# Performance work log

Measured on AMD Instinct MI355X. Metric: run time of the kernel, lower is better.

Reference implementation:

```python
import jax, jax.numpy as jnp
import numpy as np

B, S, T, D, H_HEADS = 2, 2048, 2048, 1024, 16
HD = D // H_HEADS
EPS = 1e-5


def _ln(x, g, b):
    m = jnp.mean(x, axis=-1, keepdims=True)
    v = jnp.mean(jnp.square(x - m), axis=-1, keepdims=True)
    return g * (x - m) * jax.lax.rsqrt(v + EPS) + b


def _mha(xq, xkv, Wq, bq, Wk, bk, Wv, bv, Wo, bo, causal):
    Bq, Lq, _ = xq.shape
    Lk = xkv.shape[1]
    q = (xq @ Wq + bq).reshape(Bq, Lq, H_HEADS, HD)
    k = (xkv @ Wk + bk).reshape(Bq, Lk, H_HEADS, HD)
    v = (xkv @ Wv + bv).reshape(Bq, Lk, H_HEADS, HD)
    scores = jnp.einsum('bqhd,bkhd->bhqk', q, k) / jnp.sqrt(jnp.asarray(HD, q.dtype))
    if causal:
        mask = jnp.tril(jnp.ones((Lq, Lk), dtype=bool))
        scores = jnp.where(mask, scores, jnp.asarray(-1e9, scores.dtype))
    p = jax.nn.softmax(scores, axis=-1)
    o = jnp.einsum('bhqk,bkhd->bqhd', p, v).reshape(Bq, Lq, D)
    return o @ Wo + bo


def setup_inputs() -> dict:
    key = jax.random.key(0)
    ks = jax.random.split(key, 24)
    s = 0.02
    def w(i):
        return jax.random.normal(ks[i], (D, D), jnp.float32) * s
    inp = {
        'S0': jax.random.normal(ks[20], (B, S, D), jnp.float32),
        'H': jax.random.normal(ks[21], (B, T, D), jnp.float32),
        'Wq1': w(0), 'bq1': jnp.zeros((D,)), 'Wk1': w(1), 'bk1': jnp.zeros((D,)),
        'Wv1': w(2), 'bv1': jnp.zeros((D,)), 'Wo1': w(3), 'bo1': jnp.zeros((D,)),
        'ln1_g': jnp.ones((D,)), 'ln1_b': jnp.zeros((D,)),
        'Wq2': w(4), 'bq2': jnp.zeros((D,)), 'Wk2': w(5), 'bk2': jnp.zeros((D,)),
        'Wv2': w(6), 'bv2': jnp.zeros((D,)), 'Wo2': w(7), 'bo2': jnp.zeros((D,)),
        'ln2_g': jnp.ones((D,)), 'ln2_b': jnp.zeros((D,)),
        'Wf': w(8), 'bf': jnp.zeros((D,)),
        'ln3_g': jnp.ones((D,)), 'ln3_b': jnp.zeros((D,)),
    }
    return inp


def reference(S0, H, Wq1, bq1, Wk1, bk1, Wv1, bv1, Wo1, bo1, ln1_g, ln1_b,
              Wq2, bq2, Wk2, bk2, Wv2, bv2, Wo2, bo2, ln2_g, ln2_b,
              Wf, bf, ln3_g, ln3_b):
    # masked (causal) self-attention + add&norm
    a1 = _mha(S0, S0, Wq1, bq1, Wk1, bk1, Wv1, bv1, Wo1, bo1, causal=True)
    S1 = _ln(S0 + a1, ln1_g, ln1_b)
    # cross-attention over encoder output H + add&norm
    a2 = _mha(S1, H, Wq2, bq2, Wk2, bk2, Wv2, bv2, Wo2, bo2, causal=False)
    S2 = _ln(S1 + a2, ln2_g, ln2_b)
    # FFN (single Linear) + add&norm
    S3 = _ln(S2 + (S2 @ Wf + bf), ln3_g, ln3_b)
    return S3
```

## Files before the change

kernel.cpp:

```cpp
#include <hip/hip_runtime.h>
#include <hip/hip_bf16.h>
#include <cstdint>
#include <cstddef>


#define D_DIM 1024
#define SEQ   2048
#define NHEAD 16
#define HDIM  64
#define MROWS 4096

typedef __attribute__((ext_vector_type(8)))  short bf16x8;
typedef __attribute__((ext_vector_type(4)))  float f32x4;
typedef __attribute__((ext_vector_type(16))) float f32x16;
typedef __attribute__((ext_vector_type(4)))  unsigned int u32x4;

static __device__ __forceinline__ short f2bf(float x) {
    __hip_bfloat16 h = __float2bfloat16(x);
    return *reinterpret_cast<short*>(&h);
}

static __device__ __forceinline__ unsigned int cvtpk(float lo, float hi2) {
    unsigned int r;
    asm("v_cvt_pk_bf16_f32 %0, %1, %2" : "=v"(r) : "v"(lo), "v"(hi2));
    return r;
}

#define GLOAD_LDS16(g, l)                                                     \
    __builtin_amdgcn_global_load_lds(                                         \
        (const __attribute__((address_space(1))) unsigned int*)(g),           \
        (__attribute__((address_space(3))) unsigned int*)(l), 16, 0, 0)

struct WPtrs { const float* p[9]; };

__global__ __launch_bounds__(256) void transpose_conv_kernel(
    WPtrs wp, short* __restrict__ Wt)
{
    __shared__ float tl[64][65];
    const int t = threadIdx.x;
    const float* src = wp.p[blockIdx.z];
    short* dst = Wt + (size_t)blockIdx.z * D_DIM * D_DIM;
    const int r0 = blockIdx.x * 64;
    const int c0 = blockIdx.y * 64;
    #pragma unroll
    for (int i = 0; i < 4; ++i) {
        int row = i * 16 + (t >> 4);
        int col = (t & 15) * 4;
        float4 v = *(const float4*)(src + (size_t)(r0 + row) * D_DIM + c0 + col);
        tl[row][col + 0] = v.x; tl[row][col + 1] = v.y;
        tl[row][col + 2] = v.z; tl[row][col + 3] = v.w;
    }
    __syncthreads();
    #pragma unroll
    for (int i = 0; i < 4; ++i) {
        int nrow = i * 16 + (t >> 4);
        int kcol = (t & 15) * 4;
        ushort4 o;
        o.x = (unsigned short)f2bf(tl[kcol + 0][nrow]);
        o.y = (unsigned short)f2bf(tl[kcol + 1][nrow]);
        o.z = (unsigned short)f2bf(tl[kcol + 2][nrow]);
        o.w = (unsigned short)f2bf(tl[kcol + 3][nrow]);
        *(ushort4*)(dst + (size_t)(c0 + nrow) * D_DIM + r0 + kcol) = o;
    }
}

__global__ __launch_bounds__(256) void conv2_kernel(
    const float* __restrict__ s0, const float* __restrict__ hx,
    short* __restrict__ d0, short* __restrict__ d1)
{
    const bool second = blockIdx.x >= 2048;
    const float* src = second ? hx : s0;
    short* dst = second ? d1 : d0;
    size_t i = ((size_t)(blockIdx.x - (second ? 2048 : 0)) * 256 + threadIdx.x) * 8;
    float4 a = *(const float4*)(src + i);
    float4 b = *(const float4*)(src + i + 4);
    bf16x8 o;
    o[0] = f2bf(a.x); o[1] = f2bf(a.y); o[2] = f2bf(a.z); o[3] = f2bf(a.w);
    o[4] = f2bf(b.x); o[5] = f2bf(b.y); o[6] = f2bf(b.z); o[7] = f2bf(b.w);
    *(bf16x8*)(dst + i) = o;
}

__global__ __launch_bounds__(256) void bias_concat_kernel(
    const float* __restrict__ bq1, const float* __restrict__ bk1,
    const float* __restrict__ bv1, const float* __restrict__ bk2,
    const float* __restrict__ bv2, float* __restrict__ cb1,
    float* __restrict__ cb2)
{
    const int i = blockIdx.x * 256 + threadIdx.x;
    if      (i < 1024) cb1[i] = bq1[i];
    else if (i < 2048) cb1[i] = bk1[i - 1024];
    else if (i < 3072) cb1[i] = bv1[i - 2048];
    else if (i < 4096) cb2[i - 3072] = bk2[i - 3072];
    else               cb2[i - 3072] = bv2[i - 4096];
}

__device__ __forceinline__ void gemm_qkv_body(
    short* __restrict__ As_, short* __restrict__ Bs_,
    const short* __restrict__ A, const short* __restrict__ Bt,
    const float* __restrict__ bias,
    short* __restrict__ Qh, short* __restrict__ Kh, short* __restrict__ Vh,
    int col0, float qscale, int bx, int by)
{
    const int t = threadIdx.x;
    const int wave = t >> 6, lane = t & 63;
    const int wm = wave >> 1, wn = wave & 1;
    const int m0 = bx * 128, n0 = by * 128;
    const int l15 = lane & 15, l4 = lane >> 4;
    const int lrow = lane >> 2, lcol = (lane & 3) * 8;
    f32x4 acc[4][4] = {};
    for (int k0 = 0; k0 < D_DIM; k0 += 32) {
        __syncthreads();
        #pragma unroll
        for (int c = 0; c < 2; ++c) {
            int chunk = wave + c * 4;
            int row = chunk * 16 + lrow;
            GLOAD_LDS16(A  + (size_t)(m0 + row) * D_DIM + k0 + lcol,
                        As_ + chunk * 512 + lane * 8);
            GLOAD_LDS16(Bt + (size_t)(n0 + row) * D_DIM + k0 + lcol,
                        Bs_ + chunk * 512 + lane * 8);
        }
        __syncthreads();
        bf16x8 af[4], bfr[4];
        const int kq = l4 * 8;
        #pragma unroll
        for (int i = 0; i < 4; ++i)
            af[i] = *(const bf16x8*)&As_[(wm * 64 + i * 16 + l15) * 32 + kq];
        #pragma unroll
        for (int j = 0; j < 4; ++j)
            bfr[j] = *(const bf16x8*)&Bs_[(wn * 64 + j * 16 + l15) * 32 + kq];
        #pragma unroll
        for (int i = 0; i < 4; ++i)
            #pragma unroll
            for (int j = 0; j < 4; ++j)
                acc[i][j] = __builtin_amdgcn_mfma_f32_16x16x32_bf16(
                    af[i], bfr[j], acc[i][j], 0, 0, 0);
    }
    const int rbase = m0 + wm * 64;
    const int cbase = n0 + wn * 64;
    float bv[4];
    #pragma unroll
    for (int j = 0; j < 4; ++j) bv[j] = bias[cbase + j * 16 + l15];
    #pragma unroll
    for (int i = 0; i < 4; ++i) {
        #pragma unroll
        for (int r = 0; r < 4; ++r) {
            const int grow = rbase + i * 16 + l4 * 4 + r;
            const int b = grow >> 11, s = grow & 2047;
            #pragma unroll
            for (int j = 0; j < 4; ++j) {
                const int vcol = col0 + cbase + j * 16 + l15;
                float v = acc[i][j][r] + bv[j];
                if (vcol < 1024) v *= qscale;
                short* dst = (vcol < 1024) ? Qh : ((vcol < 2048) ? Kh : Vh);
                const int h = (vcol >> 6) & 15, hd = vcol & 63;
                dst[((size_t)(b * 16 + h) * SEQ + s) * HDIM + hd] = f2bf(v);
            }
        }
    }
}

__global__ __launch_bounds__(256) void gemm_qkv_kernel(
    const short* __restrict__ A, const short* __restrict__ Bt,
    const float* __restrict__ bias,
    short* __restrict__ Qh, short* __restrict__ Kh, short* __restrict__ Vh,
    int col0, float qscale)
{
    __shared__ short lds[8192];
    gemm_qkv_body(lds, lds + 4096, A, Bt, bias, Qh, Kh, Vh,
                  col0, qscale, blockIdx.x, blockIdx.y);
}

__global__ __launch_bounds__(256) void gemm_resid_kernel(
    const short* __restrict__ A, const short* __restrict__ Bt,
    const float* __restrict__ bias, const float* __restrict__ resid,
    float* __restrict__ Cout)
{
    __shared__ short As[128 * 32];
    __shared__ short Bs[64 * 32];
    const int t = threadIdx.x;
    const int wave = t >> 6, lane = t & 63;
    const int wm = wave >> 1, wn = wave & 1;
    const int m0 = blockIdx.x * 128, n0 = blockIdx.y * 64;
    const int l15 = lane & 15, l4 = lane >> 4;
    const int lrow = lane >> 2, lcol = (lane & 3) * 8;
    f32x4 acc[4][2] = {};
    for (int k0 = 0; k0 < D_DIM; k0 += 32) {
        __syncthreads();
        #pragma unroll
        for (int c = 0; c < 2; ++c) {
            int chunk = wave + c * 4;
            int row = chunk * 16 + lrow;
            GLOAD_LDS16(A + (size_t)(m0 + row) * D_DIM + k0 + lcol,
                        As + chunk * 512 + lane * 8);
        }
        {
            int row = wave * 16 + lrow;
            GLOAD_LDS16(Bt + (size_t)(n0 + row) * D_DIM + k0 + lcol,
                        Bs + wave * 512 + lane * 8);
        }
        __syncthreads();
        bf16x8 af[4], bfr[2];
        const int kq = l4 * 8;
        #pragma unroll
        for (int i = 0; i < 4; ++i)
            af[i] = *(const bf16x8*)&As[(wm * 64 + i * 16 + l15) * 32 + kq];
        #pragma unroll
        for (int j = 0; j < 2; ++j)
            bfr[j] = *(const bf16x8*)&Bs[(wn * 32 + j * 16 + l15) * 32 + kq];
        #pragma unroll
        for (int i = 0; i < 4; ++i)
            #pragma unroll
            for (int j = 0; j < 2; ++j)
                acc[i][j] = __builtin_amdgcn_mfma_f32_16x16x32_bf16(
                    af[i], bfr[j], acc[i][j], 0, 0, 0);
    }
    const int rbase = m0 + wm * 64;
    const int cbase = n0 + wn * 32;
    float bv[2];
    #pragma unroll
    for (int j = 0; j < 2; ++j) bv[j] = bias[cbase + j * 16 + l15];
    #pragma unroll
    for (int i = 0; i < 4; ++i) {
        #pragma unroll
        for (int r = 0; r < 4; ++r) {
            const int grow = rbase + i * 16 + l4 * 4 + r;
            #pragma unroll
            for (int j = 0; j < 2; ++j) {
                const int gcol = cbase + j * 16 + l15;
                float v = acc[i][j][r] + bv[j]
                        + resid[(size_t)grow * D_DIM + gcol];
                Cout[(size_t)grow * D_DIM + gcol] = v;
            }
        }
    }
}

template<bool CAUSAL>
__device__ __forceinline__ void attn_body(
    char* ldsb,
    const short* __restrict__ Qh, const short* __restrict__ Kh,
    const short* __restrict__ Vh, short* __restrict__ O, const int id)
{
    const int t = threadIdx.x, wave = t >> 6, lane = t & 63;
    const int q_own = lane & 31, hi = lane >> 5;
    const int bh = ((id & 7) << 2) | ((id >> 3) & 3);
    const int qsel = id >> 5;
    const int b = bh >> 4, h = bh & 15;
    const short* Qp = Qh + (size_t)bh * SEQ * HDIM;
    const short* Kp = Kh + (size_t)bh * SEQ * HDIM;
    const short* Vp = Vh + (size_t)bh * SEQ * HDIM;
    short* Op = O + (size_t)b * SEQ * D_DIM + h * HDIM;

    const int ksrc = (t & 7) ^ ((t >> 3) & 7);
    const int vr2 = (t & 31) * 2, vg = (t >> 5) * 8;
    const int swz = (q_own & 7) << 3;

    const int npm = CAUSAL ? 2 : 1;
    for (int pm = 0; pm < npm; ++pm) {
        const int qt = CAUSAL ? (pm == 0 ? qsel : 15 - qsel) : qsel;
        const int q0 = qt * 128;
        const int qw = q0 + wave * 32;

        bf16x8 qf[4];
        #pragma unroll
        for (int s = 0; s < 4; ++s)
            qf[s] = *(const bf16x8*)(Qp + (size_t)(qw + q_own) * HDIM
                                     + s * 16 + hi * 8);

        int qkb[4], pvb[8], vwb[8], kgb;
        #pragma unroll
        for (int s = 0; s < 4; ++s)
            qkb[s] = q_own * 128 + 2 * ((s * 16 + hi * 8) ^ swz);
        #pragma unroll
        for (int ks = 0; ks < 8; ++ks)
            pvb[ks] = 32768 + q_own * 256 + 2 * ((ks * 16 + hi * 8) ^ swz);
        #pragma unroll
        for (int j = 0; j < 8; ++j)
            vwb[j] = 32768 + (vg + j) * 256 + 2 * (vr2 ^ (j << 3));
        kgb = t * 16;

        f32x16 oacc[2] = {};
        float m_ = -3e38f, l_ = 0.f;
        const int nkt = CAUSAL ? (qt + 1) : (SEQ / 128);

        bf16x8 va0, vb0, va1, vb1;

        if (pm) __syncthreads();

        #pragma unroll
        for (int c = 0; c < 4; ++c) {
            const int row = c * 32 + (t >> 3);
            GLOAD_LDS16(Kp + (size_t)row * HDIM + ksrc * 8,
                        ldsb + kgb + c * 4096);
        }
        va0 = *(const bf16x8*)(Vp + (size_t)vr2 * HDIM + vg);
        vb0 = *(const bf16x8*)(Vp + (size_t)(vr2 + 1) * HDIM + vg);
        va1 = *(const bf16x8*)(Vp + (size_t)(64 + vr2) * HDIM + vg);
        vb1 = *(const bf16x8*)(Vp + (size_t)(65 + vr2) * HDIM + vg);
        #pragma unroll
        for (int j = 0; j < 8; ++j) {
            unsigned int p0 = ((unsigned int)(unsigned short)vb0[j] << 16)
                            | (unsigned short)va0[j];
            unsigned int p1 = ((unsigned int)(unsigned short)vb1[j] << 16)
                            | (unsigned short)va1[j];
            *(unsigned int*)(ldsb + vwb[j])       = p0;
            *(unsigned int*)(ldsb + vwb[j] + 128) = p1;
        }
        __syncthreads();
        kgb ^= 16384;
        #pragma unroll
        for (int j = 0; j < 8; ++j) vwb[j] ^= 16384;

        for (int kt = 0; kt < nkt; ++kt) {
            const int kbase = kt * 128;
            const bool have_next = (kt + 1 < nkt);

            if (have_next) {
                #pragma unroll
                for (int c = 0; c < 4; ++c) {
                    const int row = kbase + 128 + c * 32 + (t >> 3);
                    GLOAD_LDS16(Kp + (size_t)row * HDIM + ksrc * 8,
                                ldsb + kgb + c * 4096);
                }
                va0 = *(const bf16x8*)(Vp + (size_t)(kbase + 128 + vr2) * HDIM + vg);
                vb0 = *(const bf16x8*)(Vp + (size_t)(kbase + 129 + vr2) * HDIM + vg);
                va1 = *(const bf16x8*)(Vp + (size_t)(kbase + 192 + vr2) * HDIM + vg);
                vb1 = *(const bf16x8*)(Vp + (size_t)(kbase + 193 + vr2) * HDIM + vg);
            }

            f32x16 sc[4] = {};
            __builtin_amdgcn_s_setprio(1);
            #pragma unroll
            for (int kt2 = 0; kt2 < 4; ++kt2) {
                #pragma unroll
                for (int s = 0; s < 4; ++s) {
                    bf16x8 kf = *(const bf16x8*)(ldsb + qkb[s] + kt2 * 4096);
                    sc[kt2] = __builtin_amdgcn_mfma_f32_32x32x16_bf16(
                        kf, qf[s], sc[kt2], 0, 0, 0);
                }
            }
            __builtin_amdgcn_s_setprio(0);

            if (CAUSAL && (kbase + 127 > qw)) {
                #pragma unroll
                for (int kt2 = 0; kt2 < 4; ++kt2)
                    #pragma unroll
                    for (int rr = 0; rr < 16; ++rr) {
                        const int k = kbase + kt2 * 32
                                    + (rr & 3) + 8 * (rr >> 2) + 4 * hi;
                        if (k > qw + q_own) sc[kt2][rr] = -1e30f;
                    }
            }

            float km[4];
            #pragma unroll
            for (int kt2 = 0; kt2 < 4; ++kt2) {
                float t0 = fmaxf(fmaxf(sc[kt2][0],  sc[kt2][1]),  sc[kt2][2]);
                float t1 = fmaxf(fmaxf(sc[kt2][3],  sc[kt2][4]),  sc[kt2][5]);
                float t2 = fmaxf(fmaxf(sc[kt2][6],  sc[kt2][7]),  sc[kt2][8]);
                float t3 = fmaxf(fmaxf(sc[kt2][9],  sc[kt2][10]), sc[kt2][11]);
                float t4 = fmaxf(fmaxf(sc[kt2][12], sc[kt2][13]), sc[kt2][14]);
                float u  = fmaxf(fmaxf(t0, t1), t2);
                float v  = fmaxf(fmaxf(t3, t4), sc[kt2][15]);
                km[kt2] = fmaxf(u, v);
            }
            float pmax = fmaxf(fmaxf(fmaxf(km[0], km[1]), km[2]), km[3]);
            pmax = fmaxf(pmax, __shfl_xor(pmax, 32));

            if (!__all(pmax - m_ <= 8.0f)) {
                const float mnew = fmaxf(m_, pmax);
                const float corr = exp2f(m_ - mnew);
                l_ *= corr;
                #pragma unroll
                for (int ht = 0; ht < 2; ++ht)
                    #pragma unroll
                    for (int rr = 0; rr < 16; ++rr)
                        oacc[ht][rr] *= corr;
                m_ = mnew;
            }

            float s_own = 0.f;
            #pragma unroll
            for (int kt2 = 0; kt2 < 4; ++kt2) {
                float t0 = 0.f, t1 = 0.f, t2 = 0.f, t3 = 0.f;
                #pragma unroll
                for (int rr = 0; rr < 4; ++rr) {
                    float a  = exp2f(sc[kt2][rr]      - m_);
                    float b2 = exp2f(sc[kt2][4 + rr]  - m_);
                    float c  = exp2f(sc[kt2][8 + rr]  - m_);
                    float d  = exp2f(sc[kt2][12 + rr] - m_);
                    sc[kt2][rr] = a;      t0 += a;
                    sc[kt2][4 + rr] = b2; t1 += b2;
                    sc[kt2][8 + rr] = c;  t2 += c;
                    sc[kt2][12 + rr] = d; t3 += d;
                }
                s_own += (t0 + t1) + (t2 + t3);
            }
            l_ += s_own + __shfl_xor(s_own, 32);

            u32x4 paw[8];
            #pragma unroll
            for (int kt2 = 0; kt2 < 4; ++kt2) {
                unsigned int w0a = cvtpk(sc[kt2][0],  sc[kt2][1]);
                unsigned int w0b = cvtpk(sc[kt2][2],  sc[kt2][3]);
                unsigned int w1a = cvtpk(sc[kt2][4],  sc[kt2][5]);
                unsigned int w1b = cvtpk(sc[kt2][6],  sc[kt2][7]);
                unsigned int w2a = cvtpk(sc[kt2][8],  sc[kt2][9]);
                unsigned int w2b = cvtpk(sc[kt2][10], sc[kt2][11]);
                unsigned int w3a = cvtpk(sc[kt2][12], sc[kt2][13]);
                unsigned int w3b = cvtpk(sc[kt2][14], sc[kt2][15]);
                asm("v_permlane32_swap_b32 %0, %1" : "+v"(w0a), "+v"(w1a));
                asm("v_permlane32_swap_b32 %0, %1" : "+v"(w0b), "+v"(w1b));
                asm("v_permlane32_swap_b32 %0, %1" : "+v"(w2a), "+v"(w3a));
                asm("v_permlane32_swap_b32 %0, %1" : "+v"(w2b), "+v"(w3b));
                paw[kt2 * 2 + 0][0] = w0a; paw[kt2 * 2 + 0][1] = w0b;
                paw[kt2 * 2 + 0][2] = w1a; paw[kt2 * 2 + 0][3] = w1b;
                paw[kt2 * 2 + 1][0] = w2a; paw[kt2 * 2 + 1][1] = w2b;
                paw[kt2 * 2 + 1][2] = w3a; paw[kt2 * 2 + 1][3] = w3b;
            }

            __builtin_amdgcn_s_setprio(1);
            #pragma unroll
            for (int ht = 0; ht < 2; ++ht) {
                #pragma unroll
                for (int ks = 0; ks < 8; ++ks) {
                    bf16x8 vf = *(const bf16x8*)(ldsb + pvb[ks] + ht * 8192);
                    union { u32x4 u; bf16x8 bv8; } pc;
                    pc.u = paw[ks];
                    oacc[ht] = __builtin_amdgcn_mfma_f32_32x32x16_bf16(
                        vf, pc.bv8, oacc[ht], 0, 0, 0);
                }
            }
            __builtin_amdgcn_s_setprio(0);

            if (have_next) {
                #pragma unroll
                for (int j = 0; j < 8; ++j) {
                    unsigned int p0 = ((unsigned int)(unsigned short)vb0[j] << 16)
                                    | (unsigned short)va0[j];
                    unsigned int p1 = ((unsigned int)(unsigned short)vb1[j] << 16)
                                    | (unsigned short)va1[j];
                    *(unsigned int*)(ldsb + vwb[j])       = p0;
                    *(unsigned int*)(ldsb + vwb[j] + 128) = p1;
                }
                __syncthreads();
            }
            kgb ^= 16384;
            #pragma unroll
            for (int s = 0; s < 4; ++s) qkb[s] ^= 16384;
            #pragma unroll
            for (int ks = 0; ks < 8; ++ks) pvb[ks] ^= 16384;
            #pragma unroll
            for (int j = 0; j < 8; ++j) vwb[j] ^= 16384;
        }

        const float inv = 1.0f / l_;
        const int grow = qw + q_own;
        #pragma unroll
        for (int ht = 0; ht < 2; ++ht)
            #pragma unroll
            for (int j = 0; j < 4; ++j) {
                ushort4 o;
                o.x = (unsigned short)f2bf(oacc[ht][4 * j + 0] * inv);
                o.y = (unsigned short)f2bf(oacc[ht][4 * j + 1] * inv);
                o.z = (unsigned short)f2bf(oacc[ht][4 * j + 2] * inv);
                o.w = (unsigned short)f2bf(oacc[ht][4 * j + 3] * inv);
                *(ushort4*)&Op[(size_t)grow * D_DIM + ht * 32 + 8 * j + 4 * hi] = o;
            }
    }
}

template<bool CAUSAL>
__global__ __launch_bounds__(256, 2) void attn_mfma_kernel(
    const short* __restrict__ Qh, const short* __restrict__ Kh,
    const short* __restrict__ Vh, short* __restrict__ O)
{
    __shared__ short lds[32768];
    attn_body<CAUSAL>((char*)lds, Qh, Kh, Vh, O, blockIdx.x);
}

__global__ __launch_bounds__(256, 2) void fused_cattn_kv2_kernel(
    const short* __restrict__ Qh, const short* __restrict__ Kh,
    const short* __restrict__ Vh, short* __restrict__ O,
    const short* __restrict__ A2, const short* __restrict__ Bt2,
    const float* __restrict__ bias2,
    short* __restrict__ Kh2, short* __restrict__ Vh2)
{
    __shared__ short lds[32768];
    if (blockIdx.x < 256) {
        attn_body<true>((char*)lds, Qh, Kh, Vh, O, blockIdx.x);
    } else {
        const int bx2 = blockIdx.x - 256;
        gemm_qkv_body(lds, lds + 4096, A2, Bt2, bias2,
                      nullptr, Kh2, Vh2, 1024, 1.0f, bx2 & 31, bx2 >> 5);
    }
}

__global__ __launch_bounds__(256) void ln_kernel(
    const float* __restrict__ X, const float* __restrict__ g,
    const float* __restrict__ bb, float* __restrict__ outf,
    short* __restrict__ outb)
{
    const int row = blockIdx.x;
    const int t = threadIdx.x;
    const float* x = X + (size_t)row * D_DIM;
    float4 v = *(const float4*)(x + (t << 2));
    float s  = v.x + v.y + v.z + v.w;
    float sq = v.x * v.x + v.y * v.y + v.z * v.z + v.w * v.w;
    #pragma unroll
    for (int off = 1; off < 64; off <<= 1) {
        s  += __shfl_xor(s, off);
        sq += __shfl_xor(sq, off);
    }
    __shared__ float ss[4], ssq[4];
    const int wid = t >> 6, lane = t & 63;
    if (lane == 0) { ss[wid] = s; ssq[wid] = sq; }
    __syncthreads();
    s  = ss[0] + ss[1] + ss[2] + ss[3];
    sq = ssq[0] + ssq[1] + ssq[2] + ssq[3];
    const float mean = s * (1.0f / 1024.0f);
    const float var  = sq * (1.0f / 1024.0f) - mean * mean;
    const float inv  = rsqrtf(var + 1e-5f);
    float4 gv = *(const float4*)(g  + (t << 2));
    float4 bv = *(const float4*)(bb + (t << 2));
    float4 o;
    o.x = gv.x * (v.x - mean) * inv + bv.x;
    o.y = gv.y * (v.y - mean) * inv + bv.y;
    o.z = gv.z * (v.z - mean) * inv + bv.z;
    o.w = gv.w * (v.w - mean) * inv + bv.w;
    if (outf) *(float4*)(outf + (size_t)row * D_DIM + (t << 2)) = o;
    if (outb) {
        ushort4 ob;
        ob.x = (unsigned short)f2bf(o.x); ob.y = (unsigned short)f2bf(o.y);
        ob.z = (unsigned short)f2bf(o.z); ob.w = (unsigned short)f2bf(o.w);
        *(ushort4*)(outb + (size_t)row * D_DIM + (t << 2)) = ob;
    }
}

extern "C" void kernel_launch(void* const* d_in, const int* in_sizes, int n_in,
                              void* d_out, int out_size, void* d_ws, size_t ws_size,
                              hipStream_t stream)
{
    (void)in_sizes; (void)n_in; (void)out_size; (void)ws_size;
    const float* S0f = (const float*)d_in[0];
    const float* Hf  = (const float*)d_in[1];
    const float* bq1 = (const float*)d_in[3];
    const float* bk1 = (const float*)d_in[5];
    const float* bv1 = (const float*)d_in[7];
    const float* bo1 = (const float*)d_in[9];
    const float* g1  = (const float*)d_in[10]; const float* b1 = (const float*)d_in[11];
    const float* bq2 = (const float*)d_in[13];
    const float* bk2 = (const float*)d_in[15];
    const float* bv2 = (const float*)d_in[17];
    const float* bo2 = (const float*)d_in[19];
    const float* g2  = (const float*)d_in[20]; const float* b2 = (const float*)d_in[21];
    const float* bff = (const float*)d_in[23];
    const float* g3  = (const float*)d_in[24]; const float* b3 = (const float*)d_in[25];

    char* ws = (char*)d_ws;
    size_t off = 0;
    auto alloc = [&](size_t bytes) { char* p = ws + off; off += (bytes + 255) & ~(size_t)255; return p; };
    short* Wt   = (short*)alloc((size_t)9 * D_DIM * D_DIM * 2);
    short* bS0  = (short*)alloc((size_t)MROWS * D_DIM * 2);
    short* bH   = (short*)alloc((size_t)MROWS * D_DIM * 2);
    short* Qhb  = (short*)alloc((size_t)MROWS * D_DIM * 2);
    short* Khb  = (short*)alloc((size_t)MROWS * D_DIM * 2);
    short* Vhb  = (short*)alloc((size_t)MROWS * D_DIM * 2);
    short* Khb2 = (short*)alloc((size_t)MROWS * D_DIM * 2);
    short* Vhb2 = (short*)alloc((size_t)MROWS * D_DIM * 2);
    short* bAO  = (short*)alloc((size_t)MROWS * D_DIM * 2);
    float* X    = (float*)alloc((size_t)MROWS * D_DIM * 4);
    short* bSx  = (short*)alloc((size_t)MROWS * D_DIM * 2);
    float* cb1  = (float*)alloc(3072 * 4);
    float* cb2  = (float*)alloc(2048 * 4);

    const size_t WSTRIDE = (size_t)D_DIM * D_DIM;
    const float QSCALE = 0.125f * 1.44269504088896f;

    WPtrs wp;
    wp.p[0] = (const float*)d_in[2];
    wp.p[1] = (const float*)d_in[4];
    wp.p[2] = (const float*)d_in[6];
    wp.p[3] = (const float*)d_in[8];
    wp.p[4] = (const float*)d_in[12];
    wp.p[5] = (const float*)d_in[14];
    wp.p[6] = (const float*)d_in[16];
    wp.p[7] = (const float*)d_in[18];
    wp.p[8] = (const float*)d_in[22];
    transpose_conv_kernel<<<dim3(16, 16, 9), 256, 0, stream>>>(wp, Wt);

    conv2_kernel<<<4096, 256, 0, stream>>>(S0f, Hf, bS0, bH);
    bias_concat_kernel<<<20, 256, 0, stream>>>(bq1, bk1, bv1, bk2, bv2, cb1, cb2);

    const dim3 blk(256);
    const dim3 attn_grid_f(512);
    const dim3 resid_grid(32, 16);

    gemm_qkv_kernel<<<dim3(32, 24), blk, 0, stream>>>(
        bS0, Wt, cb1, Qhb, Khb, Vhb, 0, QSCALE);
    fused_cattn_kv2_kernel<<<dim3(768), blk, 0, stream>>>(
        Qhb, Khb, Vhb, bAO, bH, Wt + 5 * WSTRIDE, cb2, Khb2, Vhb2);
    gemm_resid_kernel<<<resid_grid, blk, 0, stream>>>(
        bAO, Wt + 3 * WSTRIDE, bo1, S0f, X);
    ln_kernel<<<MROWS, blk, 0, stream>>>(X, g1, b1, X, bSx);

    gemm_qkv_kernel<<<dim3(32, 8), blk, 0, stream>>>(
        bSx, Wt + 4 * WSTRIDE, bq2, Qhb, Khb, Vhb, 0, QSCALE);
    attn_mfma_kernel<false><<<attn_grid_f, blk, 0, stream>>>(
        Qhb, Khb2, Vhb2, bAO);
    gemm_resid_kernel<<<resid_grid, blk, 0, stream>>>(
        bAO, Wt + 7 * WSTRIDE, bo2, X, X);
    ln_kernel<<<MROWS, blk, 0, stream>>>(X, g2, b2, X, bSx);

    gemm_resid_kernel<<<resid_grid, blk, 0, stream>>>(
        bSx, Wt + 8 * WSTRIDE, bff, X, X);
    ln_kernel<<<MROWS, blk, 0, stream>>>(X, g3, b3, (float*)d_out, nullptr);
}
```

Baseline: 277.5 us.

## Fold max subtraction into MFMA init and compute row sums via ones-MFMA

The score accumulators are now initialised to -m so the QK MFMA yields pre-shifted scores, which removes the per-element subtraction before exp2. The softmax row-sum is computed by an extra MFMA against a ones vector, fed with the same bf16 P fragments, instead of VALU adds and a cross-lane shuffle. The PV loop is interleaved across the two head-dim halves. This trades VALU work for one more MFMA per k-step, and the denominator is now summed from bf16-rounded probabilities, which slightly changes the numerics.

```diff
diff --git a/kernel.cpp b/kernel.cpp
--- a/kernel.cpp
+++ b/kernel.cpp
@@ -255,6 +255,10 @@
     const int vr2 = (t & 31) * 2, vg = (t >> 5) * 8;
     const int swz = (q_own & 7) << 3;
 
+    bf16x8 ones;
+    #pragma unroll
+    for (int j = 0; j < 8; ++j) ones[j] = (short)0x3F80;
+
     const int npm = CAUSAL ? 2 : 1;
     for (int pm = 0; pm < npm; ++pm) {
         const int qt = CAUSAL ? (pm == 0 ? qsel : 15 - qsel) : qsel;
@@ -280,7 +284,8 @@
         kgb = t * 16;
 
         f32x16 oacc[2] = {};
-        float m_ = -3e38f, l_ = 0.f;
+        f32x16 lsum = {};
+        float m_ = 0.0f;
         const int nkt = CAUSAL ? (qt + 1) : (SEQ / 128);
 
         bf16x8 va0, vb0, va1, vb1;
@@ -328,7 +333,11 @@
                 vb1 = *(const bf16x8*)(Vp + (size_t)(kbase + 193 + vr2) * HDIM + vg);
             }
 
-            f32x16 sc[4] = {};
+            f32x16 minit;
+            #pragma unroll
+            for (int rr = 0; rr < 16; ++rr) minit[rr] = -m_;
+            f32x16 sc[4];
+            sc[0] = minit; sc[1] = minit; sc[2] = minit; sc[3] = minit;
             __builtin_amdgcn_s_setprio(1);
             #pragma unroll
             for (int kt2 = 0; kt2 < 4; ++kt2) {
@@ -364,39 +373,31 @@
                 float v  = fmaxf(fmaxf(t3, t4), sc[kt2][15]);
                 km[kt2] = fmaxf(u, v);
             }
-            float pmax = fmaxf(fmaxf(fmaxf(km[0], km[1]), km[2]), km[3]);
-            pmax = fmaxf(pmax, __shfl_xor(pmax, 32));
-
-            if (!__all(pmax - m_ <= 8.0f)) {
-                const float mnew = fmaxf(m_, pmax);
-                const float corr = exp2f(m_ - mnew);
-                l_ *= corr;
+            float smax = fmaxf(fmaxf(fmaxf(km[0], km[1]), km[2]), km[3]);
+            smax = fmaxf(smax, __shfl_xor(smax, 32));
+
+            if (!__all(smax <= 8.0f)) {
+                const float sp = fmaxf(smax, 0.f);
+                const float corr = exp2f(-sp);
+                lsum[0] *= corr;
                 #pragma unroll
                 for (int ht = 0; ht < 2; ++ht)
                     #pragma unroll
                     for (int rr = 0; rr < 16; ++rr)
                         oacc[ht][rr] *= corr;
-                m_ = mnew;
-            }
-
-            float s_own = 0.f;
-            #pragma unroll
-            for (int kt2 = 0; kt2 < 4; ++kt2) {
-                float t0 = 0.f, t1 = 0.f, t2 = 0.f, t3 = 0.f;
                 #pragma unroll
-                for (int rr = 0; rr < 4; ++rr) {
-                    float a  = exp2f(sc[kt2][rr]      - m_);
-                    float b2 = exp2f(sc[kt2][4 + rr]  - m_);
-                    float c  = exp2f(sc[kt2][8 + rr]  - m_);
-                    float d  = exp2f(sc[kt2][12 + rr] - m_);
-                    sc[kt2][rr] = a;      t0 += a;
-                    sc[kt2][4 + rr] = b2; t1 += b2;
-                    sc[kt2][8 + rr] = c;  t2 += c;
-                    sc[kt2][12 + rr] = d; t3 += d;
-                }
-                s_own += (t0 + t1) + (t2 + t3);
-            }
-            l_ += s_own + __shfl_xor(s_own, 32);
+                for (int kt2 = 0; kt2 < 4; ++kt2)
+                    #pragma unroll
+                    for (int rr = 0; rr < 16; ++rr)
+                        sc[kt2][rr] -= sp;
+                m_ += sp;
+            }
+
+            #pragma unroll
+            for (int kt2 = 0; kt2 < 4; ++kt2)
+                #pragma unroll
+                for (int rr = 0; rr < 16; ++rr)
+                    sc[kt2][rr] = exp2f(sc[kt2][rr]);
 
             u32x4 paw[8];
             #pragma unroll
@@ -421,15 +422,17 @@
 
             __builtin_amdgcn_s_setprio(1);
             #pragma unroll
-            for (int ht = 0; ht < 2; ++ht) {
-                #pragma unroll
-                for (int ks = 0; ks < 8; ++ks) {
-                    bf16x8 vf = *(const bf16x8*)(ldsb + pvb[ks] + ht * 8192);
-                    union { u32x4 u; bf16x8 bv8; } pc;
-                    pc.u = paw[ks];
-                    oacc[ht] = __builtin_amdgcn_mfma_f32_32x32x16_bf16(
-                        vf, pc.bv8, oacc[ht], 0, 0, 0);
-                }
+            for (int ks = 0; ks < 8; ++ks) {
+                union { u32x4 u; bf16x8 bv8; } pc;
+                pc.u = paw[ks];
+                bf16x8 vf0 = *(const bf16x8*)(ldsb + pvb[ks]);
+                oacc[0] = __builtin_amdgcn_mfma_f32_32x32x16_bf16(
+                    vf0, pc.bv8, oacc[0], 0, 0, 0);
+                bf16x8 vf1 = *(const bf16x8*)(ldsb + pvb[ks] + 8192);
+                oacc[1] = __builtin_amdgcn_mfma_f32_32x32x16_bf16(
+                    vf1, pc.bv8, oacc[1], 0, 0, 0);
+                lsum = __builtin_amdgcn_mfma_f32_32x32x16_bf16(
+                    ones, pc.bv8, lsum, 0, 0, 0);
             }
             __builtin_amdgcn_s_setprio(0);
 
@@ -454,7 +457,7 @@
             for (int j = 0; j < 8; ++j) vwb[j] ^= 16384;
         }
 
-        const float inv = 1.0f / l_;
+        const float inv = 1.0f / lsum[0];
         const int grow = qw + q_own;
         #pragma unroll
         for (int ht = 0; ht < 2; ++ht)
```

Result: no change. 279.0 us (+0.6%).
